# Performance work log

Hardware: AMD Instinct MI355X
Metric: run time of the kernel (lower is better)

## Reference

```python
import jax, jax.numpy as jnp
import numpy as np

B, N, DIM = 32, 3136, 64
H, DH, AGENTS = 8, 8, 49
INNER = H * DH  # 64
SCALE = DH ** -0.5


def setup_inputs() -> dict:
    key = jax.random.key(0)
    ks = jax.random.split(key, 7)
    s = 0.05
    return {
        "x1": jax.random.normal(ks[0], (B, N, DIM), jnp.float32),
        "x2": jax.random.normal(ks[1], (B, N, INNER), jnp.float32),
        "Wq": jax.random.normal(ks[2], (INNER, DIM), jnp.float32) * s,   # to_q (out,in)
        "Wk": jax.random.normal(ks[3], (DIM, INNER), jnp.float32) * s,   # to_k
        "Wv": jax.random.normal(ks[4], (DIM, INNER), jnp.float32) * s,   # to_v
        "Wo": jax.random.normal(ks[5], (2 * DIM, 2 * DIM), jnp.float32) * s,  # to_out linear
        "bo": jax.random.normal(ks[6], (2 * DIM,), jnp.float32) * s,
    }


def _split_heads(t):
    # (b, n, h*d) -> (b, h, n, d)
    b, n, hd = t.shape
    return t.reshape(b, n, H, hd // H).transpose(0, 2, 1, 3)


def reference(x1, x2, Wq, Wk, Wv, Wo, bo):
    b, n, _ = x1.shape
    q = x1 @ Wq.T                      # (b, n, 64)
    k = x2 @ Wk.T                      # (b, n, dim=64)
    v = x2 @ Wv.T
    # AdaptiveAvgPool2d((49, dim)): n % 49 == 0 and channel 64->64 is identity,
    # so pooling is an exact block mean over the sequence axis.
    agent = q.reshape(b, AGENTS, n // AGENTS, q.shape[-1]).mean(axis=2)  # (b, 49, 64)

    agent_h = _split_heads(agent)      # (b, h, 49, d)
    q1 = _split_heads(q)               # (b, h, n, d)
    k_h = _split_heads(k)
    v_h = _split_heads(v)

    # stage 0: agent tokens attend over keys/values (dropout is identity at eval)
    dots0 = jnp.einsum('bhid,bhjd->bhij', agent_h, k_h) * SCALE   # (b,h,49,n)
    attn0 = jax.nn.softmax(dots0, axis=-1)
    out0 = jnp.einsum('bhij,bhjd->bhid', attn0, v_h)              # (b,h,49,d)

    # stage 1: queries attend over agent tokens
    dots1 = jnp.einsum('bhid,bhjd->bhij', q1, agent_h) * SCALE    # (b,h,n,49)
    attn1 = jax.nn.softmax(dots1, axis=-1)
    out1 = jnp.einsum('bhij,bhjd->bhid', attn1, out0)             # (b,h,n,d)

    out1 = out1.transpose(0, 2, 1, 3).reshape(b, n, -1)           # (b,n,64)
    out1 = jnp.concatenate([out1, x1], axis=-1)                   # (b,n,128)
    return out1 @ Wo.T + bo
```

## Files before the change

kernel.cpp:

```cpp
#include <hip/hip_runtime.h>
#include <hip/hip_bf16.h>

#define NB 32
#define NSEQ 3136
#define NDIM 64
#define NH 8
#define NAG 49
#define SPLIT 4

static constexpr float kScale = 0.35355339059327378f;
static constexpr float kLog2e = 1.4426950408889634f;

typedef unsigned short us;
typedef __attribute__((ext_vector_type(8))) __bf16 bf16x8;
typedef __attribute__((ext_vector_type(2))) _Float16 f16x2;
typedef __attribute__((ext_vector_type(4))) _Float16 f16x4;
typedef __attribute__((ext_vector_type(8))) _Float16 f16x8;
typedef __attribute__((ext_vector_type(4))) float f32x4;
typedef __attribute__((ext_vector_type(2))) float f32x2;

__device__ __forceinline__ float fexp2(float x) {
#if __has_builtin(__builtin_amdgcn_exp2f)
  return __builtin_amdgcn_exp2f(x);
#else
  return exp2f(x);
#endif
}

__device__ __forceinline__ float frcp(float x) {
#if __has_builtin(__builtin_amdgcn_rcpf)
  return __builtin_amdgcn_rcpf(x);
#else
  return 1.f / x;
#endif
}

__device__ __forceinline__ unsigned pk2(float a, float b) {
#if __has_builtin(__builtin_amdgcn_cvt_pkrtz)
  return __builtin_bit_cast(unsigned, __builtin_amdgcn_cvt_pkrtz(a, b));
#else
  f16x2 v = {(_Float16)a, (_Float16)b};
  return __builtin_bit_cast(unsigned, v);
#endif
}

__global__ __launch_bounds__(256) void prep_kernel(
    const float* __restrict__ Wq, const float* __restrict__ Wk,
    const float* __restrict__ Wv, const float* __restrict__ Wo,
    __bf16* __restrict__ wq, __bf16* __restrict__ wk, __bf16* __restrict__ wv,
    __bf16* __restrict__ wo, us* __restrict__ kvhk, us* __restrict__ vt) {
  int i = blockIdx.x * 256 + threadIdx.x;
  wo[i] = (__bf16)Wo[i];
  if (i < 4096) { wq[i] = (__bf16)Wq[i]; wk[i] = (__bf16)Wk[i]; wv[i] = (__bf16)Wv[i]; }
  if (i < 32) kvhk[(size_t)NB * NH * NSEQ * 8 + i] = 0;
  const us one = 0x3C00;
  for (size_t j = i; j < (size_t)NB * NH * NSEQ; j += 16384) {
    size_t bh = j / NSEQ, tok = j - bh * NSEQ;
    vt[(bh * 9 + 8) * NSEQ + tok] = one;
  }
}

__global__ __launch_bounds__(256, 4) void qkv_agent_kernel(
    const float* __restrict__ x1, const float* __restrict__ x2,
    const float* __restrict__ Wq, const __bf16* __restrict__ wk,
    const __bf16* __restrict__ wv, us* __restrict__ kvhk, us* __restrict__ vt,
    us* __restrict__ agf16) {
  __shared__ __align__(16) __bf16 xb[64][72];
  __shared__ __align__(16) float red[4][64];
  __shared__ __align__(16) float marr[64];
  const int a = blockIdx.x, b = blockIdx.y, t = threadIdx.x;
  const int i64 = t & 63, cb = t >> 6;
  const int w = cb, lr = (t >> 4) & 3, lc = t & 15;

  bf16x8 ak0 = *(const bf16x8*)(wk + (size_t)(w * 16 + lc) * NDIM + lr * 8);
  bf16x8 ak1 = *(const bf16x8*)(wk + (size_t)(w * 16 + lc) * NDIM + 32 + lr * 8);
  bf16x8 av0 = *(const bf16x8*)(wv + (size_t)(w * 16 + lc) * NDIM + lr * 8);
  bf16x8 av1 = *(const bf16x8*)(wv + (size_t)(w * 16 + lc) * NDIM + 32 + lr * 8);

  {
    const float4* s2 = (const float4*)(x2 + ((size_t)(b * NSEQ) + a * 64 + i64) * NDIM + cb * 16);
    float4 v0 = s2[0], v1 = s2[1], v2 = s2[2], v3 = s2[3];
    bf16x8 p0, p1;
    p0[0]=(__bf16)v0.x; p0[1]=(__bf16)v0.y; p0[2]=(__bf16)v0.z; p0[3]=(__bf16)v0.w;
    p0[4]=(__bf16)v1.x; p0[5]=(__bf16)v1.y; p0[6]=(__bf16)v1.z; p0[7]=(__bf16)v1.w;
    p1[0]=(__bf16)v2.x; p1[1]=(__bf16)v2.y; p1[2]=(__bf16)v2.z; p1[3]=(__bf16)v2.w;
    p1[4]=(__bf16)v3.x; p1[5]=(__bf16)v3.y; p1[6]=(__bf16)v3.z; p1[7]=(__bf16)v3.w;
    *(bf16x8*)&xb[i64][cb * 16] = p0; *(bf16x8*)&xb[i64][cb * 16 + 8] = p1;
  }
  {
    const float* xc = x1 + ((size_t)(b * NSEQ) + a * 64 + cb * 16) * NDIM + i64;
    float cs = 0.f;
#pragma unroll
    for (int i = 0; i < 16; ++i) cs += xc[i * NDIM];
    red[cb][i64] = cs;
  }
  __syncthreads();

  f32x4 acck[4], accv[4];
#pragma unroll
  for (int i = 0; i < 4; ++i) {
    acck[i] = (f32x4){0.f, 0.f, 0.f, 0.f};
    accv[i] = (f32x4){0.f, 0.f, 0.f, 0.f};
  }
#pragma unroll
  for (int nt = 0; nt < 4; ++nt) {
    bf16x8 x0 = *(const bf16x8*)&xb[nt * 16 + lc][lr * 8];
    bf16x8 x1f = *(const bf16x8*)&xb[nt * 16 + lc][32 + lr * 8];
    acck[nt] = __builtin_amdgcn_mfma_f32_16x16x32_bf16(ak0, x0, acck[nt], 0, 0, 0);
    acck[nt] = __builtin_amdgcn_mfma_f32_16x16x32_bf16(ak1, x1f, acck[nt], 0, 0, 0);
    accv[nt] = __builtin_amdgcn_mfma_f32_16x16x32_bf16(av0, x0, accv[nt], 0, 0, 0);
    accv[nt] = __builtin_amdgcn_mfma_f32_16x16x32_bf16(av1, x1f, accv[nt], 0, 0, 0);
  }
  const int head = 2 * w + (lr >> 1), sb = (lr & 1) * 4;
  {
    _Float16* kdst = (_Float16*)kvhk + ((size_t)(b * NH + head) * NSEQ) * 8 + sb;
#pragma unroll
    for (int nt = 0; nt < 4; ++nt) {
      const int tok = a * 64 + nt * 16 + lc;
      f16x4 pk4;
      pk4[0]=(_Float16)acck[nt][0]; pk4[1]=(_Float16)acck[nt][1];
      pk4[2]=(_Float16)acck[nt][2]; pk4[3]=(_Float16)acck[nt][3];
      *(f16x4*)(kdst + (size_t)tok * 8) = pk4;
    }
  }
  __syncthreads();

  _Float16 (*vtile)[72] = (_Float16(*)[72])xb;
  {
    const int f0 = w * 16 + lr * 4;
#pragma unroll
    for (int nt = 0; nt < 4; ++nt) {
      const int tok = nt * 16 + lc;
#pragma unroll
      for (int j = 0; j < 4; ++j) vtile[f0 + j][tok] = (_Float16)accv[nt][j];
    }
  }
  if (t < 64) marr[t] = red[0][t] + red[1][t] + red[2][t] + red[3][t];
  __syncthreads();

  {
    const int r = t >> 2, p = t & 3;
    _Float16* drow = (_Float16*)vt +
        ((size_t)(b * NH + (r >> 3)) * 9 + (r & 7)) * NSEQ + a * 64 + p * 16;
    f16x8 v0 = *(const f16x8*)&vtile[r][p * 16];
    f16x8 v1 = *(const f16x8*)&vtile[r][p * 16 + 8];
    *(f16x8*)drow = v0;
    *(f16x8*)(drow + 8) = v1;
  }
  if (t < 64) {
    const float4* wqr = (const float4*)(Wq + (size_t)t * NDIM);
    const float4* mm = (const float4*)marr;
    float s0 = 0.f;
#pragma unroll
    for (int i = 0; i < 16; ++i) {
      float4 wv4 = wqr[i], m4 = mm[i];
      s0 += wv4.x * m4.x + wv4.y * m4.y + wv4.z * m4.z + wv4.w * m4.w;
    }
    const float val = s0 * (kScale * kLog2e / 64.f);
    ((_Float16*)agf16)[(((size_t)b * NH + (t >> 3)) * NAG + a) * 8 + (t & 7)] =
        (_Float16)val;
  }
}

__global__ __launch_bounds__(256, 4) void stage0_kernel(
    const us* __restrict__ kvhk, const us* __restrict__ vt,
    const us* __restrict__ agf16, float* __restrict__ pvs_z) {
  __shared__ _Float16 pshuf[4][4][16][40];
  __shared__ float redS[64][12];
  const int h = blockIdx.x, b = blockIdx.y, z = blockIdx.z;
  const int t = threadIdx.x, l = t & 63, w = t >> 6;
  for (int i = t; i < 64 * 12; i += 256) (&redS[0][0])[i] = 0.f;

  const int lg = l >> 4, lm = l & 15;
  const size_t bh = (size_t)b * NH + h;
  const us* kb = kvhk + bh * ((size_t)NSEQ * 8);
  const us* vb = vt + bh * ((size_t)9 * NSEQ);
  const us* ab = agf16 + bh * (NAG * 8);

  f16x8 ba[4];
#pragma unroll
  for (int at = 0; at < 4; ++at) {
    f16x8 v = (f16x8)(_Float16)0.0f;
    if (lg == 0) {
      int row = at * 16 + lm; if (row > 48) row = 48;
      v = *(const f16x8*)(ab + row * 8);
    }
    ba[at] = v;
  }
  const us* vrow = vb + (size_t)((lm > 8) ? 8 : lm) * NSEQ + lg * 8;

  f32x4 accPV[4];
#pragma unroll
  for (int i = 0; i < 4; ++i) accPV[i] = (f32x4){0.f, 0.f, 0.f, 0.f};

  _Float16* ps = &pshuf[w][0][0][0];
  const int iw = z * 4 + w;
  __syncthreads();

  f16x8 aK0, aK1, bV;
  aK0 = *(const f16x8*)(kb + ((size_t)iw * 32 + lm) * 8 + lg * 8);
  aK1 = *(const f16x8*)(kb + ((size_t)iw * 32 + 16 + lm) * 8 + lg * 8);
  bV  = *(const f16x8*)(vrow + iw * 32);

  for (int c = iw; c < 98; c += 16) {
    f16x8 nK0, nK1, nV;
    const int cn = c + 16;
    if (cn < 98) {
      nK0 = *(const f16x8*)(kb + ((size_t)cn * 32 + lm) * 8 + lg * 8);
      nK1 = *(const f16x8*)(kb + ((size_t)cn * 32 + 16 + lm) * 8 + lg * 8);
      nV  = *(const f16x8*)(vrow + cn * 32);
    }
#pragma unroll
    for (int at = 0; at < 4; ++at) {
      f32x4 s0 = __builtin_amdgcn_mfma_f32_16x16x32_f16(
          aK0, ba[at], (f32x4){0.f, 0.f, 0.f, 0.f}, 0, 0, 0);
      f32x4 s1 = __builtin_amdgcn_mfma_f32_16x16x32_f16(
          aK1, ba[at], (f32x4){0.f, 0.f, 0.f, 0.f}, 0, 0, 0);
      unsigned p00 = pk2(fexp2(s0[0]), fexp2(s0[1]));
      unsigned p01 = pk2(fexp2(s0[2]), fexp2(s0[3]));
      unsigned p10 = pk2(fexp2(s1[0]), fexp2(s1[1]));
      unsigned p11 = pk2(fexp2(s1[2]), fexp2(s1[3]));
      unsigned long long q0 = ((unsigned long long)p01 << 32) | p00;
      unsigned long long q1 = ((unsigned long long)p11 << 32) | p10;
      _Float16* prow = ps + (size_t)(at * 16 + lm) * 40;
      *(unsigned long long*)(prow + lg * 4) = q0;
      *(unsigned long long*)(prow + 16 + lg * 4) = q1;
    }
#pragma unroll
    for (int at = 0; at < 4; ++at) {
      f16x8 aP = *(const f16x8*)(ps + (size_t)(at * 16 + lm) * 40 + lg * 8);
      accPV[at] = __builtin_amdgcn_mfma_f32_16x16x32_f16(aP, bV, accPV[at], 0, 0, 0);
    }
    aK0 = nK0; aK1 = nK1; bV = nV;
  }

  if (lm < 9) {
#pragma unroll
    for (int at = 0; at < 4; ++at)
#pragma unroll
      for (int jj = 0; jj < 4; ++jj) {
        const int ag = at * 16 + lg * 4 + jj;
        if (ag < NAG) atomicAdd(&redS[ag][lm], accPV[at][jj]);
      }
  }
  __syncthreads();
  float* pz = pvs_z + ((size_t)z * (NB * NH) + bh) * (NAG * 12);
  for (int i = t; i < NAG * 9; i += 256) {
    pz[(i / 9) * 12 + (i % 9)] = redS[i / 9][i % 9];
  }
}

__global__ __launch_bounds__(64) void aofin_kernel(
    const float* __restrict__ pvs_z, us* __restrict__ pvtF) {
  const int h = blockIdx.x, b = blockIdx.y, t = threadIdx.x;
  const size_t bh = (size_t)b * NH + h;
  f32x4 pv0 = (f32x4){0.f,0.f,0.f,0.f}, pv1 = (f32x4){0.f,0.f,0.f,0.f};
  float den = 0.f;
  if (t < NAG) {
#pragma unroll
    for (int zz = 0; zz < SPLIT; ++zz) {
      const float* pp = pvs_z + (((size_t)zz * (NB * NH) + bh) * NAG + t) * 12;
      pv0 += *(const f32x4*)pp;
      pv1 += *(const f32x4*)(pp + 4);
      den += pp[8];
    }
  }
  float inv = (t < NAG) ? frcp(den) : 0.f;
  us* col = pvtF + bh * 1024 + t;
  _Float16 v0 = (_Float16)(pv0[0]*inv), v1 = (_Float16)(pv0[1]*inv);
  _Float16 v2 = (_Float16)(pv0[2]*inv), v3 = (_Float16)(pv0[3]*inv);
  _Float16 v4 = (_Float16)(pv1[0]*inv), v5 = (_Float16)(pv1[1]*inv);
  _Float16 v6 = (_Float16)(pv1[2]*inv), v7 = (_Float16)(pv1[3]*inv);
  col[0*64] = __builtin_bit_cast(us, v0); col[1*64] = __builtin_bit_cast(us, v1);
  col[2*64] = __builtin_bit_cast(us, v2); col[3*64] = __builtin_bit_cast(us, v3);
  col[4*64] = __builtin_bit_cast(us, v4); col[5*64] = __builtin_bit_cast(us, v5);
  col[6*64] = __builtin_bit_cast(us, v6); col[7*64] = __builtin_bit_cast(us, v7);
  col[8*64] = (t < NAG) ? (us)0x3C00 : (us)0;
#pragma unroll
  for (int f = 9; f < 16; ++f) col[f*64] = 0;
}

__global__ __launch_bounds__(512, 6) void stage1_out_kernel(
    const float* __restrict__ x1, const __bf16* __restrict__ wq,
    const us* __restrict__ agf16, const us* __restrict__ pvtF,
    const __bf16* __restrict__ wo, const float* __restrict__ bo,
    float* __restrict__ out) {
  __shared__ __align__(16) __bf16 xa[64][72];
  __shared__ __align__(16) us qcat[64][72];
  __shared__ __align__(16) _Float16 pW[8][16][72];
  const int tile = blockIdx.x, b = blockIdx.y;
  const int t = threadIdx.x, tokl = t & 63, h = t >> 6;
  const int w = h, lane = t & 63, lr = (lane >> 4) & 3, lc = lane & 15;
  const int mtile = w & 3, thalf = w >> 2;
  const size_t bh = (size_t)b * NH + w;

  bf16x8 wqf0 = *(const bf16x8*)(wq + (size_t)(mtile * 16 + lc) * NDIM + lr * 8);
  bf16x8 wqf1 = *(const bf16x8*)(wq + (size_t)(mtile * 16 + lc) * NDIM + 32 + lr * 8);

  f16x8 ba[4];
#pragma unroll
  for (int at = 0; at < 4; ++at) {
    f16x8 v = (f16x8)(_Float16)0.0f;
    if (lr == 0) {
      int row = at * 16 + lc; if (row > 48) row = 48;
      v = *(const f16x8*)(agf16 + bh * (NAG * 8) + row * 8);
    }
    ba[at] = v;
  }
  const us* pvb = pvtF + bh * 1024;
  f16x8 pvB0 = *(const f16x8*)(pvb + lc * 64 + lr * 8);
  f16x8 pvB1 = *(const f16x8*)(pvb + lc * 64 + 32 + lr * 8);

  {
    const float4* src = (const float4*)(x1 + ((size_t)b * NSEQ + tile * 64 + tokl) * NDIM + h * 8);
    float4 v0 = src[0], v1 = src[1];
    bf16x8 p;
    p[0]=(__bf16)v0.x; p[1]=(__bf16)v0.y; p[2]=(__bf16)v0.z; p[3]=(__bf16)v0.w;
    p[4]=(__bf16)v1.x; p[5]=(__bf16)v1.y; p[6]=(__bf16)v1.z; p[7]=(__bf16)v1.w;
    *(bf16x8*)&xa[tokl][h * 8] = p;
  }
  __syncthreads();

  {
    f32x4 aq[2];
    aq[0] = (f32x4){0.f,0.f,0.f,0.f}; aq[1] = (f32x4){0.f,0.f,0.f,0.f};
#pragma unroll
    for (int nt = 0; nt < 2; ++nt) {
      bf16x8 bx0 = *(const bf16x8*)&xa[thalf * 32 + nt * 16 + lc][lr * 8];
      bf16x8 bx1 = *(const bf16x8*)&xa[thalf * 32 + nt * 16 + lc][32 + lr * 8];
      aq[nt] = __builtin_amdgcn_mfma_f32_16x16x32_bf16(wqf0, bx0, aq[nt], 0, 0, 0);
      aq[nt] = __builtin_amdgcn_mfma_f32_16x16x32_bf16(wqf1, bx1, aq[nt], 0, 0, 0);
    }
#pragma unroll
    for (int nt = 0; nt < 2; ++nt) {
      f16x4 pk;
      pk[0]=(_Float16)aq[nt][0]; pk[1]=(_Float16)aq[nt][1];
      pk[2]=(_Float16)aq[nt][2]; pk[3]=(_Float16)aq[nt][3];
      *(f16x4*)&qcat[thalf * 32 + nt * 16 + lc][mtile * 16 + lr * 4] = pk;
    }
  }
  __syncthreads();

  {
    _Float16* psw = &pW[w][0][0];
    const int swz = (lc & 7) << 4;
#pragma unroll 1
    for (int g = 0; g < 4; ++g) {
      f16x8 qf = *(const f16x8*)&qcat[g * 16 + lc][w * 8];
#pragma unroll
      for (int at = 0; at < 4; ++at) {
        f32x4 sc = __builtin_amdgcn_mfma_f32_16x16x32_f16(
            ba[at], qf, (f32x4){0.f, 0.f, 0.f, 0.f}, 0, 0, 0);
        unsigned u0 = pk2(fexp2(sc[0]), fexp2(sc[1]));
        unsigned u1 = pk2(fexp2(sc[2]), fexp2(sc[3]));
        unsigned long long q = ((unsigned long long)u1 << 32) | u0;
        *(unsigned long long*)((char*)psw + lc * 144 + (((at * 32) | (lr * 8)) ^ swz)) = q;
      }
      f16x8 pA0 = *(const f16x8*)((char*)psw + lc * 144 + ((lr * 16) ^ swz));
      f16x8 pA1 = *(const f16x8*)((char*)psw + lc * 144 + ((64 + lr * 16) ^ swz));
      f32x4 pv = __builtin_amdgcn_mfma_f32_16x16x32_f16(pA0, pvB0,
                   (f32x4){0.f, 0.f, 0.f, 0.f}, 0, 0, 0);
      pv = __builtin_amdgcn_mfma_f32_16x16x32_f16(pA1, pvB1, pv, 0, 0, 0);
#pragma unroll
      for (int j = 0; j < 4; ++j) {
        float den = __shfl(pv[j], (lane & 48) | 8);
        if (lc < 8) {
          float val = pv[j] * frcp(den);
          *(__bf16*)&qcat[g * 16 + lr * 4 + j][w * 8 + lc] = (__bf16)val;
        }
      }
    }
  }
  bf16x8 wof[4];
#pragma unroll
  for (int ks = 0; ks < 4; ++ks)
    wof[ks] = *(const bf16x8*)(wo + (size_t)(w * 16 + lc) * 128 + ks * 32 + lr * 8);
  f32x4 bv = *(const f32x4*)(bo + w * 16 + lr * 4);
  __syncthreads();

  {
    f32x4 acc[4];
#pragma unroll
    for (int i = 0; i < 4; ++i) acc[i] = (f32x4){0.f,0.f,0.f,0.f};
#pragma unroll
    for (int ks = 0; ks < 4; ++ks) {
#pragma unroll
      for (int nt = 0; nt < 4; ++nt) {
        bf16x8 bx = (ks < 2) ? *(const bf16x8*)&qcat[nt * 16 + lc][ks * 32 + lr * 8]
                             : *(const bf16x8*)&xa[nt * 16 + lc][(ks - 2) * 32 + lr * 8];
        acc[nt] = __builtin_amdgcn_mfma_f32_16x16x32_bf16(wof[ks], bx, acc[nt], 0, 0, 0);
      }
    }
#pragma unroll
    for (int nt = 0; nt < 4; ++nt) {
      f32x4 v = acc[nt] + bv;
      float* dst = out + ((size_t)b * NSEQ + tile * 64 + nt * 16 + lc) * 128 + w * 16 + lr * 4;
      *(f32x4*)dst = v;
    }
  }
}

extern "C" void kernel_launch(void* const* d_in, const int* in_sizes, int n_in,
                              void* d_out, int out_size, void* d_ws, size_t ws_size,
                              hipStream_t stream) {
  (void)in_sizes; (void)n_in; (void)out_size; (void)ws_size;
  const float* x1 = (const float*)d_in[0];
  const float* x2 = (const float*)d_in[1];
  const float* Wq = (const float*)d_in[2];
  const float* Wk = (const float*)d_in[3];
  const float* Wv = (const float*)d_in[4];
  const float* Wo = (const float*)d_in[5];
  const float* bo = (const float*)d_in[6];
  float* out = (float*)d_out;

  us* vt = (us*)d_ws;
  us* kvhk = vt + (size_t)NB * NH * 9 * NSEQ;
  us* agf16 = kvhk + (size_t)NB * NH * NSEQ * 8 + 32;
  float* pvs_z = (float*)(agf16 + (size_t)NB * NH * NAG * 8);
  us* pvtF = (us*)(pvs_z + (size_t)SPLIT * NB * NH * NAG * 12);
  __bf16* wq_bf = (__bf16*)(pvtF + (size_t)NB * NH * 1024);
  __bf16* wk_bf = wq_bf + 4096;
  __bf16* wv_bf = wk_bf + 4096;
  __bf16* wo_bf = wv_bf + 4096;

  prep_kernel<<<dim3(64), 256, 0, stream>>>(Wq, Wk, Wv, Wo, wq_bf, wk_bf, wv_bf,
                                            wo_bf, kvhk, vt);
  qkv_agent_kernel<<<dim3(NAG, NB), 256, 0, stream>>>(x1, x2, Wq, wk_bf, wv_bf,
                                                      kvhk, vt, agf16);
  stage0_kernel<<<dim3(NH, NB, SPLIT), 256, 0, stream>>>(kvhk, vt, agf16, pvs_z);
  aofin_kernel<<<dim3(NH, NB), 64, 0, stream>>>(pvs_z, pvtF);
  stage1_out_kernel<<<dim3(NAG, NB), 512, 0, stream>>>(x1, wq_bf, agf16, pvtF,
                                                       wo_bf, bo, out);
}
```

Before: 79.48 us.

## Fuse K/V projection into stage-0 attention and drop weight prep kernel

K and V are now projected per 64-token tile and consumed straight from LDS inside a fused kv_stage0 kernel that computes exp-scores and PV partials per tile. This avoids writing and re-reading the K/V intermediates through global memory and removes the separate prep kernel by converting weights to bf16 on load. A new agent_x1 kernel computes the agent means and writes a bf16 tiled copy of x1 for the final stage. The cost is a large partial buffer (49 tiles per batch-head) that aofin must reduce serially, plus redundant weight conversion in every block.

Result: no change. 80.57 us (+1.4%).

```diff
diff --git a/kernel.cpp b/kernel.cpp
--- a/kernel.cpp
+++ b/kernel.cpp
@@ -6,7 +6,6 @@
 #define NDIM 64
 #define NH 8
 #define NAG 49
-#define SPLIT 4
 
 static constexpr float kScale = 0.35355339059327378f;
 static constexpr float kLog2e = 1.4426950408889634f;
@@ -17,7 +16,6 @@
 typedef __attribute__((ext_vector_type(4))) _Float16 f16x4;
 typedef __attribute__((ext_vector_type(8))) _Float16 f16x8;
 typedef __attribute__((ext_vector_type(4))) float f32x4;
-typedef __attribute__((ext_vector_type(2))) float f32x2;
 
 __device__ __forceinline__ float fexp2(float x) {
 #if __has_builtin(__builtin_amdgcn_exp2f)
@@ -44,38 +42,76 @@
 #endif
 }
 
-__global__ __launch_bounds__(256) void prep_kernel(
-    const float* __restrict__ Wq, const float* __restrict__ Wk,
-    const float* __restrict__ Wv, const float* __restrict__ Wo,
-    __bf16* __restrict__ wq, __bf16* __restrict__ wk, __bf16* __restrict__ wv,
-    __bf16* __restrict__ wo, us* __restrict__ kvhk, us* __restrict__ vt) {
-  int i = blockIdx.x * 256 + threadIdx.x;
-  wo[i] = (__bf16)Wo[i];
-  if (i < 4096) { wq[i] = (__bf16)Wq[i]; wk[i] = (__bf16)Wk[i]; wv[i] = (__bf16)Wv[i]; }
-  if (i < 32) kvhk[(size_t)NB * NH * NSEQ * 8 + i] = 0;
-  const us one = 0x3C00;
-  for (size_t j = i; j < (size_t)NB * NH * NSEQ; j += 16384) {
-    size_t bh = j / NSEQ, tok = j - bh * NSEQ;
-    vt[(bh * 9 + 8) * NSEQ + tok] = one;
-  }
-}
-
-__global__ __launch_bounds__(256, 4) void qkv_agent_kernel(
-    const float* __restrict__ x1, const float* __restrict__ x2,
-    const float* __restrict__ Wq, const __bf16* __restrict__ wk,
-    const __bf16* __restrict__ wv, us* __restrict__ kvhk, us* __restrict__ vt,
-    us* __restrict__ agf16) {
+__device__ __forceinline__ bf16x8 ldw8(const float* W, int row, int c0, int ld) {
+  const float4* p = (const float4*)(W + (size_t)row * ld + c0);
+  float4 v0 = p[0], v1 = p[1];
+  bf16x8 r;
+  r[0]=(__bf16)v0.x; r[1]=(__bf16)v0.y; r[2]=(__bf16)v0.z; r[3]=(__bf16)v0.w;
+  r[4]=(__bf16)v1.x; r[5]=(__bf16)v1.y; r[6]=(__bf16)v1.z; r[7]=(__bf16)v1.w;
+  return r;
+}
+
+__global__ __launch_bounds__(256) void agent_x1_kernel(
+    const float* __restrict__ x1, const float* __restrict__ Wq,
+    us* __restrict__ x1bf, us* __restrict__ agf16) {
+  __shared__ float red[4][64];
+  __shared__ float marr[64];
+  const int a = blockIdx.x, b = blockIdx.y, t = threadIdx.x;
+  const int i64 = t & 63, cb = t >> 6;
+
+  {
+    const float4* s1 = (const float4*)(x1 + ((size_t)(b * NSEQ) + a * 64 + i64) * NDIM + cb * 16);
+    float4 v0 = s1[0], v1 = s1[1], v2 = s1[2], v3 = s1[3];
+    bf16x8 p0, p1;
+    p0[0]=(__bf16)v0.x; p0[1]=(__bf16)v0.y; p0[2]=(__bf16)v0.z; p0[3]=(__bf16)v0.w;
+    p0[4]=(__bf16)v1.x; p0[5]=(__bf16)v1.y; p0[6]=(__bf16)v1.z; p0[7]=(__bf16)v1.w;
+    p1[0]=(__bf16)v2.x; p1[1]=(__bf16)v2.y; p1[2]=(__bf16)v2.z; p1[3]=(__bf16)v2.w;
+    p1[4]=(__bf16)v3.x; p1[5]=(__bf16)v3.y; p1[6]=(__bf16)v3.z; p1[7]=(__bf16)v3.w;
+    __bf16* dst = (__bf16*)x1bf;
+    *(bf16x8*)(dst + ((((size_t)b * NAG + a) * 8 + cb * 2) * 64 + i64) * 8) = p0;
+    *(bf16x8*)(dst + ((((size_t)b * NAG + a) * 8 + cb * 2 + 1) * 64 + i64) * 8) = p1;
+  }
+  {
+    const float* xc = x1 + ((size_t)(b * NSEQ) + a * 64 + cb * 16) * NDIM + i64;
+    float cs = 0.f;
+#pragma unroll
+    for (int i = 0; i < 16; ++i) cs += xc[i * NDIM];
+    red[cb][i64] = cs;
+  }
+  __syncthreads();
+  if (t < 64) marr[t] = red[0][t] + red[1][t] + red[2][t] + red[3][t];
+  __syncthreads();
+  if (t < 64) {
+    const float4* wqr = (const float4*)(Wq + (size_t)t * NDIM);
+    const float4* mm = (const float4*)marr;
+    float s0 = 0.f;
+#pragma unroll
+    for (int i = 0; i < 16; ++i) {
+      float4 wv4 = wqr[i], m4 = mm[i];
+      s0 += wv4.x * m4.x + wv4.y * m4.y + wv4.z * m4.z + wv4.w * m4.w;
+    }
+    const float val = s0 * (kScale * kLog2e / 64.f);
+    ((_Float16*)agf16)[(((size_t)b * NH + (t >> 3)) * NAG + a) * 8 + (t & 7)] =
+        (_Float16)val;
+  }
+}
+
+__global__ __launch_bounds__(256) void kv_stage0_kernel(
+    const float* __restrict__ x2, const float* __restrict__ Wk,
+    const float* __restrict__ Wv, const us* __restrict__ agf16,
+    float* __restrict__ pvp) {
   __shared__ __align__(16) __bf16 xb[64][72];
-  __shared__ __align__(16) float red[4][64];
-  __shared__ __align__(16) float marr[64];
+  __shared__ __align__(16) _Float16 klds[4][64][24];
+  __shared__ __align__(16) _Float16 vlds[4][18][72];
+  __shared__ __align__(16) _Float16 plds[4][64][40];
   const int a = blockIdx.x, b = blockIdx.y, t = threadIdx.x;
   const int i64 = t & 63, cb = t >> 6;
   const int w = cb, lr = (t >> 4) & 3, lc = t & 15;
 
-  bf16x8 ak0 = *(const bf16x8*)(wk + (size_t)(w * 16 + lc) * NDIM + lr * 8);
-  bf16x8 ak1 = *(const bf16x8*)(wk + (size_t)(w * 16 + lc) * NDIM + 32 + lr * 8);
-  bf16x8 av0 = *(const bf16x8*)(wv + (size_t)(w * 16 + lc) * NDIM + lr * 8);
-  bf16x8 av1 = *(const bf16x8*)(wv + (size_t)(w * 16 + lc) * NDIM + 32 + lr * 8);
+  bf16x8 ak0 = ldw8(Wk, w * 16 + lc, lr * 8, NDIM);
+  bf16x8 ak1 = ldw8(Wk, w * 16 + lc, 32 + lr * 8, NDIM);
+  bf16x8 av0 = ldw8(Wv, w * 16 + lc, lr * 8, NDIM);
+  bf16x8 av1 = ldw8(Wv, w * 16 + lc, 32 + lr * 8, NDIM);
 
   {
     const float4* s2 = (const float4*)(x2 + ((size_t)(b * NSEQ) + a * 64 + i64) * NDIM + cb * 16);
@@ -87,13 +123,6 @@
     p1[4]=(__bf16)v3.x; p1[5]=(__bf16)v3.y; p1[6]=(__bf16)v3.z; p1[7]=(__bf16)v3.w;
     *(bf16x8*)&xb[i64][cb * 16] = p0; *(bf16x8*)&xb[i64][cb * 16 + 8] = p1;
   }
-  {
-    const float* xc = x1 + ((size_t)(b * NSEQ) + a * 64 + cb * 16) * NDIM + i64;
-    float cs = 0.f;
-#pragma unroll
-    for (int i = 0; i < 16; ++i) cs += xc[i * NDIM];
-    red[cb][i64] = cs;
-  }
   __syncthreads();
 
   f32x4 acck[4], accv[4];
@@ -111,180 +140,107 @@
     accv[nt] = __builtin_amdgcn_mfma_f32_16x16x32_bf16(av0, x0, accv[nt], 0, 0, 0);
     accv[nt] = __builtin_amdgcn_mfma_f32_16x16x32_bf16(av1, x1f, accv[nt], 0, 0, 0);
   }
-  const int head = 2 * w + (lr >> 1), sb = (lr & 1) * 4;
-  {
-    _Float16* kdst = (_Float16*)kvhk + ((size_t)(b * NH + head) * NSEQ) * 8 + sb;
-#pragma unroll
-    for (int nt = 0; nt < 4; ++nt) {
-      const int tok = a * 64 + nt * 16 + lc;
-      f16x4 pk4;
-      pk4[0]=(_Float16)acck[nt][0]; pk4[1]=(_Float16)acck[nt][1];
-      pk4[2]=(_Float16)acck[nt][2]; pk4[3]=(_Float16)acck[nt][3];
-      *(f16x4*)(kdst + (size_t)tok * 8) = pk4;
-    }
-  }
-  __syncthreads();
-
-  _Float16 (*vtile)[72] = (_Float16(*)[72])xb;
-  {
-    const int f0 = w * 16 + lr * 4;
-#pragma unroll
-    for (int nt = 0; nt < 4; ++nt) {
-      const int tok = nt * 16 + lc;
-#pragma unroll
-      for (int j = 0; j < 4; ++j) vtile[f0 + j][tok] = (_Float16)accv[nt][j];
-    }
-  }
-  if (t < 64) marr[t] = red[0][t] + red[1][t] + red[2][t] + red[3][t];
-  __syncthreads();
-
-  {
-    const int r = t >> 2, p = t & 3;
-    _Float16* drow = (_Float16*)vt +
-        ((size_t)(b * NH + (r >> 3)) * 9 + (r & 7)) * NSEQ + a * 64 + p * 16;
-    f16x8 v0 = *(const f16x8*)&vtile[r][p * 16];
-    f16x8 v1 = *(const f16x8*)&vtile[r][p * 16 + 8];
-    *(f16x8*)drow = v0;
-    *(f16x8*)(drow + 8) = v1;
-  }
-  if (t < 64) {
-    const float4* wqr = (const float4*)(Wq + (size_t)t * NDIM);
-    const float4* mm = (const float4*)marr;
-    float s0 = 0.f;
-#pragma unroll
-    for (int i = 0; i < 16; ++i) {
-      float4 wv4 = wqr[i], m4 = mm[i];
-      s0 += wv4.x * m4.x + wv4.y * m4.y + wv4.z * m4.z + wv4.w * m4.w;
-    }
-    const float val = s0 * (kScale * kLog2e / 64.f);
-    ((_Float16*)agf16)[(((size_t)b * NH + (t >> 3)) * NAG + a) * 8 + (t & 7)] =
-        (_Float16)val;
-  }
-}
-
-__global__ __launch_bounds__(256, 4) void stage0_kernel(
-    const us* __restrict__ kvhk, const us* __restrict__ vt,
-    const us* __restrict__ agf16, float* __restrict__ pvs_z) {
-  __shared__ _Float16 pshuf[4][4][16][40];
-  __shared__ float redS[64][12];
-  const int h = blockIdx.x, b = blockIdx.y, z = blockIdx.z;
-  const int t = threadIdx.x, l = t & 63, w = t >> 6;
-  for (int i = t; i < 64 * 12; i += 256) (&redS[0][0])[i] = 0.f;
-
-  const int lg = l >> 4, lm = l & 15;
-  const size_t bh = (size_t)b * NH + h;
-  const us* kb = kvhk + bh * ((size_t)NSEQ * 8);
-  const us* vb = vt + bh * ((size_t)9 * NSEQ);
-  const us* ab = agf16 + bh * (NAG * 8);
-
-  f16x8 ba[4];
-#pragma unroll
-  for (int at = 0; at < 4; ++at) {
-    f16x8 v = (f16x8)(_Float16)0.0f;
-    if (lg == 0) {
-      int row = at * 16 + lm; if (row > 48) row = 48;
-      v = *(const f16x8*)(ab + row * 8);
-    }
-    ba[at] = v;
-  }
-  const us* vrow = vb + (size_t)((lm > 8) ? 8 : lm) * NSEQ + lg * 8;
-
-  f32x4 accPV[4];
-#pragma unroll
-  for (int i = 0; i < 4; ++i) accPV[i] = (f32x4){0.f, 0.f, 0.f, 0.f};
-
-  _Float16* ps = &pshuf[w][0][0][0];
-  const int iw = z * 4 + w;
-  __syncthreads();
-
-  f16x8 aK0, aK1, bV;
-  aK0 = *(const f16x8*)(kb + ((size_t)iw * 32 + lm) * 8 + lg * 8);
-  aK1 = *(const f16x8*)(kb + ((size_t)iw * 32 + 16 + lm) * 8 + lg * 8);
-  bV  = *(const f16x8*)(vrow + iw * 32);
-
-  for (int c = iw; c < 98; c += 16) {
-    f16x8 nK0, nK1, nV;
-    const int cn = c + 16;
-    if (cn < 98) {
-      nK0 = *(const f16x8*)(kb + ((size_t)cn * 32 + lm) * 8 + lg * 8);
-      nK1 = *(const f16x8*)(kb + ((size_t)cn * 32 + 16 + lm) * 8 + lg * 8);
-      nV  = *(const f16x8*)(vrow + cn * 32);
-    }
+#pragma unroll
+  for (int nt = 0; nt < 4; ++nt) {
+    f16x4 pk4;
+    pk4[0]=(_Float16)acck[nt][0]; pk4[1]=(_Float16)acck[nt][1];
+    pk4[2]=(_Float16)acck[nt][2]; pk4[3]=(_Float16)acck[nt][3];
+    *(f16x4*)&klds[w][nt * 16 + lc][lr * 4] = pk4;
+#pragma unroll
+    for (int j = 0; j < 4; ++j)
+      vlds[w][lr * 4 + j][nt * 16 + lc] = (_Float16)accv[nt][j];
+  }
+  vlds[w][16][i64] = (_Float16)1.0f;
+
+  const size_t bh0 = (size_t)b * NH + 2 * w;
+  f16x8 ba[2][4];
+#pragma unroll
+  for (int hh = 0; hh < 2; ++hh)
 #pragma unroll
     for (int at = 0; at < 4; ++at) {
-      f32x4 s0 = __builtin_amdgcn_mfma_f32_16x16x32_f16(
-          aK0, ba[at], (f32x4){0.f, 0.f, 0.f, 0.f}, 0, 0, 0);
-      f32x4 s1 = __builtin_amdgcn_mfma_f32_16x16x32_f16(
-          aK1, ba[at], (f32x4){0.f, 0.f, 0.f, 0.f}, 0, 0, 0);
-      unsigned p00 = pk2(fexp2(s0[0]), fexp2(s0[1]));
-      unsigned p01 = pk2(fexp2(s0[2]), fexp2(s0[3]));
-      unsigned p10 = pk2(fexp2(s1[0]), fexp2(s1[1]));
-      unsigned p11 = pk2(fexp2(s1[2]), fexp2(s1[3]));
-      unsigned long long q0 = ((unsigned long long)p01 << 32) | p00;
-      unsigned long long q1 = ((unsigned long long)p11 << 32) | p10;
-      _Float16* prow = ps + (size_t)(at * 16 + lm) * 40;
-      *(unsigned long long*)(prow + lg * 4) = q0;
-      *(unsigned long long*)(prow + 16 + lg * 4) = q1;
-    }
-#pragma unroll
-    for (int at = 0; at < 4; ++at) {
-      f16x8 aP = *(const f16x8*)(ps + (size_t)(at * 16 + lm) * 40 + lg * 8);
-      accPV[at] = __builtin_amdgcn_mfma_f32_16x16x32_f16(aP, bV, accPV[at], 0, 0, 0);
-    }
-    aK0 = nK0; aK1 = nK1; bV = nV;
-  }
-
-  if (lm < 9) {
-#pragma unroll
-    for (int at = 0; at < 4; ++at)
-#pragma unroll
-      for (int jj = 0; jj < 4; ++jj) {
-        const int ag = at * 16 + lg * 4 + jj;
-        if (ag < NAG) atomicAdd(&redS[ag][lm], accPV[at][jj]);
-      }
-  }
-  __syncthreads();
-  float* pz = pvs_z + ((size_t)z * (NB * NH) + bh) * (NAG * 12);
-  for (int i = t; i < NAG * 9; i += 256) {
-    pz[(i / 9) * 12 + (i % 9)] = redS[i / 9][i % 9];
-  }
-}
-
-__global__ __launch_bounds__(64) void aofin_kernel(
-    const float* __restrict__ pvs_z, us* __restrict__ pvtF) {
+      f16x8 v = (f16x8)(_Float16)0.0f;
+      if (lr == 0) {
+        int row = at * 16 + lc; if (row > 48) row = 48;
+        v = *(const f16x8*)(agf16 + (bh0 + hh) * (NAG * 8) + row * 8);
+      }
+      ba[hh][at] = v;
+    }
+
+#pragma unroll
+  for (int hh = 0; hh < 2; ++hh) {
+    f32x4 accPV[4];
+#pragma unroll
+    for (int i = 0; i < 4; ++i) accPV[i] = (f32x4){0.f, 0.f, 0.f, 0.f};
+#pragma unroll
+    for (int half = 0; half < 2; ++half) {
+#pragma unroll
+      for (int tb = 0; tb < 2; ++tb) {
+        const int tokbase = half * 32 + tb * 16;
+        f16x8 kf = *(const f16x8*)&klds[w][tokbase + lc][hh * 8];
+#pragma unroll
+        for (int at = 0; at < 4; ++at) {
+          f32x4 sc = __builtin_amdgcn_mfma_f32_16x16x32_f16(
+              kf, ba[hh][at], (f32x4){0.f, 0.f, 0.f, 0.f}, 0, 0, 0);
+          unsigned u0 = pk2(fexp2(sc[0]), fexp2(sc[1]));
+          unsigned u1 = pk2(fexp2(sc[2]), fexp2(sc[3]));
+          unsigned long long q = ((unsigned long long)u1 << 32) | u0;
+          *(unsigned long long*)&plds[w][at * 16 + lc][tb * 16 + lr * 4] = q;
+        }
+      }
+      const int frow = (lc < 8) ? hh * 8 + lc : 16;
+      f16x8 vf = *(const f16x8*)&vlds[w][frow][half * 32 + lr * 8];
+#pragma unroll
+      for (int at = 0; at < 4; ++at) {
+        f16x8 pf = *(const f16x8*)&plds[w][at * 16 + lc][lr * 8];
+        accPV[at] = __builtin_amdgcn_mfma_f32_16x16x32_f16(pf, vf, accPV[at], 0, 0, 0);
+      }
+    }
+    if (lc < 9) {
+      float* dst = pvp + ((size_t)a * (NB * NH) + bh0 + hh) * 441;
+#pragma unroll
+      for (int at = 0; at < 4; ++at)
+#pragma unroll
+        for (int j = 0; j < 4; ++j) {
+          const int ag = at * 16 + lr * 4 + j;
+          if (ag < NAG) dst[ag * 9 + lc] = accPV[at][j];
+        }
+    }
+  }
+}
+
+__global__ __launch_bounds__(256) void aofin_kernel(
+    const float* __restrict__ pvp, us* __restrict__ pvtF) {
+  __shared__ float acc[441];
   const int h = blockIdx.x, b = blockIdx.y, t = threadIdx.x;
   const size_t bh = (size_t)b * NH + h;
-  f32x4 pv0 = (f32x4){0.f,0.f,0.f,0.f}, pv1 = (f32x4){0.f,0.f,0.f,0.f};
-  float den = 0.f;
-  if (t < NAG) {
-#pragma unroll
-    for (int zz = 0; zz < SPLIT; ++zz) {
-      const float* pp = pvs_z + (((size_t)zz * (NB * NH) + bh) * NAG + t) * 12;
-      pv0 += *(const f32x4*)pp;
-      pv1 += *(const f32x4*)(pp + 4);
-      den += pp[8];
-    }
-  }
-  float inv = (t < NAG) ? frcp(den) : 0.f;
-  us* col = pvtF + bh * 1024 + t;
-  _Float16 v0 = (_Float16)(pv0[0]*inv), v1 = (_Float16)(pv0[1]*inv);
-  _Float16 v2 = (_Float16)(pv0[2]*inv), v3 = (_Float16)(pv0[3]*inv);
-  _Float16 v4 = (_Float16)(pv1[0]*inv), v5 = (_Float16)(pv1[1]*inv);
-  _Float16 v6 = (_Float16)(pv1[2]*inv), v7 = (_Float16)(pv1[3]*inv);
-  col[0*64] = __builtin_bit_cast(us, v0); col[1*64] = __builtin_bit_cast(us, v1);
-  col[2*64] = __builtin_bit_cast(us, v2); col[3*64] = __builtin_bit_cast(us, v3);
-  col[4*64] = __builtin_bit_cast(us, v4); col[5*64] = __builtin_bit_cast(us, v5);
-  col[6*64] = __builtin_bit_cast(us, v6); col[7*64] = __builtin_bit_cast(us, v7);
-  col[8*64] = (t < NAG) ? (us)0x3C00 : (us)0;
-#pragma unroll
-  for (int f = 9; f < 16; ++f) col[f*64] = 0;
+  for (int s = t; s < 441; s += 256) {
+    float v = 0.f;
+#pragma unroll 7
+    for (int aa = 0; aa < NAG; ++aa)
+      v += pvp[((size_t)aa * (NB * NH) + bh) * 441 + s];
+    acc[s] = v;
+  }
+  __syncthreads();
+  if (t < 64) {
+    us* col = pvtF + bh * 1024 + t;
+    float inv = (t < NAG) ? frcp(acc[t * 9 + 8]) : 0.f;
+#pragma unroll
+    for (int f = 0; f < 8; ++f) {
+      float val = (t < NAG) ? acc[t * 9 + f] * inv : 0.f;
+      _Float16 hv = (_Float16)val;
+      col[f * 64] = __builtin_bit_cast(us, hv);
+    }
+    col[8 * 64] = (t < NAG) ? (us)0x3C00 : (us)0;
+#pragma unroll
+    for (int f = 9; f < 16; ++f) col[f * 64] = 0;
+  }
 }
 
 __global__ __launch_bounds__(512, 6) void stage1_out_kernel(
-    const float* __restrict__ x1, const __bf16* __restrict__ wq,
-    const us* __restrict__ agf16, const us* __restrict__ pvtF,
-    const __bf16* __restrict__ wo, const float* __restrict__ bo,
-    float* __restrict__ out) {
+    const us* __restrict__ x1bf, const float* __restrict__ x1,
+    const float* __restrict__ Wq, const us* __restrict__ agf16,
+    const us* __restrict__ pvtF, const float* __restrict__ Wo,
+    const float* __restrict__ bo, float* __restrict__ out) {
   __shared__ __align__(16) __bf16 xa[64][72];
   __shared__ __align__(16) us qcat[64][72];
   __shared__ __align__(16) _Float16 pW[8][16][72];
@@ -294,8 +250,8 @@
   const int mtile = w & 3, thalf = w >> 2;
   const size_t bh = (size_t)b * NH + w;
 
-  bf16x8 wqf0 = *(const bf16x8*)(wq + (size_t)(mtile * 16 + lc) * NDIM + lr * 8);
-  bf16x8 wqf1 = *(const bf16x8*)(wq + (size_t)(mtile * 16 + lc) * NDIM + 32 + lr * 8);
+  bf16x8 wqf0 = ldw8(Wq, mtile * 16 + lc, lr * 8, NDIM);
+  bf16x8 wqf1 = ldw8(Wq, mtile * 16 + lc, 32 + lr * 8, NDIM);
 
   f16x8 ba[4];
 #pragma unroll
@@ -312,11 +268,8 @@
   f16x8 pvB1 = *(const f16x8*)(pvb + lc * 64 + 32 + lr * 8);
 
   {
-    const float4* src = (const float4*)(x1 + ((size_t)b * NSEQ + tile * 64 + tokl) * NDIM + h * 8);
-    float4 v0 = src[0], v1 = src[1];
-    bf16x8 p;
-    p[0]=(__bf16)v0.x; p[1]=(__bf16)v0.y; p[2]=(__bf16)v0.z; p[3]=(__bf16)v0.w;
-    p[4]=(__bf16)v1.x; p[5]=(__bf16)v1.y; p[6]=(__bf16)v1.z; p[7]=(__bf16)v1.w;
+    bf16x8 p = *(const bf16x8*)((const __bf16*)x1bf +
+        ((((size_t)b * NAG + tile) * 8 + h) * 64 + tokl) * 8);
     *(bf16x8*)&xa[tokl][h * 8] = p;
   }
   __syncthreads();
@@ -374,7 +327,7 @@
   bf16x8 wof[4];
 #pragma unroll
   for (int ks = 0; ks < 4; ++ks)
-    wof[ks] = *(const bf16x8*)(wo + (size_t)(w * 16 + lc) * 128 + ks * 32 + lr * 8);
+    wof[ks] = ldw8(Wo, w * 16 + lc, ks * 32 + lr * 8, 128);
   f32x4 bv = *(const f32x4*)(bo + w * 16 + lr * 4);
   __syncthreads();
 
@@ -398,6 +351,7 @@
       *(f32x4*)dst = v;
     }
   }
+  (void)x1;
 }
 
 extern "C" void kernel_launch(void* const* d_in, const int* in_sizes, int n_in,
@@ -413,22 +367,14 @@
   const float* bo = (const float*)d_in[6];
   float* out = (float*)d_out;
 
-  us* vt = (us*)d_ws;
-  us* kvhk = vt + (size_t)NB * NH * 9 * NSEQ;
-  us* agf16 = kvhk + (size_t)NB * NH * NSEQ * 8 + 32;
-  float* pvs_z = (float*)(agf16 + (size_t)NB * NH * NAG * 8);
-  us* pvtF = (us*)(pvs_z + (size_t)SPLIT * NB * NH * NAG * 12);
-  __bf16* wq_bf = (__bf16*)(pvtF + (size_t)NB * NH * 1024);
-  __bf16* wk_bf = wq_bf + 4096;
-  __bf16* wv_bf = wk_bf + 4096;
-  __bf16* wo_bf = wv_bf + 4096;
-
-  prep_kernel<<<dim3(64), 256, 0, stream>>>(Wq, Wk, Wv, Wo, wq_bf, wk_bf, wv_bf,
-                                            wo_bf, kvhk, vt);
-  qkv_agent_kernel<<<dim3(NAG, NB), 256, 0, stream>>>(x1, x2, Wq, wk_bf, wv_bf,
-                                                      kvhk, vt, agf16);
-  stage0_kernel<<<dim3(NH, NB, SPLIT), 256, 0, stream>>>(kvhk, vt, agf16, pvs_z);
-  aofin_kernel<<<dim3(NH, NB), 64, 0, stream>>>(pvs_z, pvtF);
-  stage1_out_kernel<<<dim3(NAG, NB), 512, 0, stream>>>(x1, wq_bf, agf16, pvtF,
-                                                       wo_bf, bo, out);
-}
+  us* x1bf = (us*)d_ws;
+  us* agf16 = x1bf + (size_t)NB * NSEQ * 64;
+  float* pvp = (float*)(agf16 + (size_t)NB * NH * NAG * 8);
+  us* pvtF = (us*)(pvp + (size_t)NAG * NB * NH * 441);
+
+  agent_x1_kernel<<<dim3(NAG, NB), 256, 0, stream>>>(x1, Wq, x1bf, agf16);
+  kv_stage0_kernel<<<dim3(NAG, NB), 256, 0, stream>>>(x2, Wk, Wv, agf16, pvp);
+  aofin_kernel<<<dim3(NH, NB), 256, 0, stream>>>(pvp, pvtF);
+  stage1_out_kernel<<<dim3(NAG, NB), 512, 0, stream>>>(x1bf, x1, Wq, agf16,
+                                                       pvtF, Wo, bo, out);
+}
```
